# Kernel tuning notes

Measured on AMD Instinct MI355X. Metric: run time of the kernel, lower is better.

The kernel has to match this reference:

```python
import jax, jax.numpy as jnp
import numpy as np

B, Lq, Lk, D, H = 8, 1024, 1024, 1024, 16
HD = D // H  # 64


def rotate_half(x):
    x1, x2 = jnp.split(x, 2, axis=-1)
    return jnp.concatenate([-x2, x1], axis=-1)


def setup_inputs() -> dict:
    key = jax.random.key(0)
    ks = jax.random.split(key, 16)
    inv_freq = 1.0 / (10000.0 ** (np.arange(0, HD, 2, dtype=np.float32) / HD))
    pos = np.arange(Lk, dtype=np.float32)
    ang = pos[:, None] * inv_freq[None, :]              # [Lk, HD/2]
    emb = np.concatenate([ang, ang], axis=-1)           # [Lk, HD]
    rope_cos = jnp.broadcast_to(jnp.asarray(np.cos(emb)), (B, Lk, HD))
    rope_sin = jnp.broadcast_to(jnp.asarray(np.sin(emb)), (B, Lk, HD))
    w = lambda k: jax.random.normal(k, (D, D), jnp.float32) * 0.02
    return {
        "query": jax.random.normal(ks[0], (B, Lq, D), jnp.float32),
        "key": jax.random.normal(ks[1], (B, Lk, D), jnp.float32),
        "value": jax.random.normal(ks[2], (B, Lk, D), jnp.float32),
        "Wq": w(ks[3]), "bq": jnp.zeros((D,), jnp.float32),
        "Wk": w(ks[4]), "bk": jnp.zeros((D,), jnp.float32),
        "Wv": w(ks[5]), "bv": jnp.zeros((D,), jnp.float32),
        "Wg": w(ks[6]), "bg": jnp.ones((D,), jnp.float32),
        "Wo": w(ks[7]), "bo": jnp.zeros((D,), jnp.float32),
        "rope_cos": rope_cos,
        "rope_sin": rope_sin,
        "key_padding_mask": jnp.zeros((B, Lk), bool),  # True = padded
    }


def reference(query, key, value, Wq, bq, Wk, bk, Wv, bv, Wg, bg, Wo, bo,
              rope_cos, rope_sin, key_padding_mask):
    b, lq, d = query.shape
    lk = key.shape[1]
    h, hd = H, d // H

    def heads(x, L):  # [B,L,D] -> [B,H,L,hd]
        return x.reshape(b, L, h, hd).transpose(0, 2, 1, 3)

    Q = heads(query @ Wq.T + bq, lq)
    K = heads(key @ Wk.T + bk, lk)
    V = heads(value @ Wv.T + bv, lk)

    def rope(x, cos, sin):
        L = x.shape[2]
        c = cos[:, None, :L, :]
        s = sin[:, None, :L, :]
        return x * c + rotate_half(x) * s

    K = rope(K, rope_cos, rope_sin)
    Q = rope(Q, rope_cos, rope_sin)  # rope_on_q=True, q uses same cos/sin

    scale = 1.0 / np.sqrt(hd)
    scores = jnp.einsum('bhqd,bhkd->bhqk', Q, K) * scale
    valid = ~key_padding_mask                     # [B,Lk], True = attend
    scores = jnp.where(valid[:, None, None, :], scores, jnp.float32(-1e30))
    attn = jax.nn.softmax(scores, axis=-1)
    out = jnp.einsum('bhqk,bhkd->bhqd', attn, V)  # [B,H,Lq,hd]
    out = jnp.nan_to_num(out, nan=0.0)
    out = out.transpose(0, 2, 1, 3).reshape(b, lq, d)
    gate = jax.nn.sigmoid(query @ Wg.T + bg)
    out = (out * gate) @ Wo.T + bo
    return out
```

## Files before the change

kernel.cpp:

```cpp
#include <hip/hip_runtime.h>

using ushort  = unsigned short;
using bf16x8  = __attribute__((ext_vector_type(8))) __bf16;
using ushort8 = __attribute__((ext_vector_type(8))) unsigned short;
using f32x4   = __attribute__((ext_vector_type(4))) float;
using float4v = __attribute__((ext_vector_type(4))) float;

__device__ __forceinline__ float bf2f(ushort u) {
    union { unsigned int i; float f; } v; v.i = ((unsigned int)u) << 16; return v.f;
}
__device__ __forceinline__ ushort f2bf(float f) {
    union { float f; unsigned int i; } v; v.f = f;
    unsigned int r = v.i + 0x7FFFu + ((v.i >> 16) & 1u);
    return (ushort)(r >> 16);
}
__device__ __forceinline__ bf16x8 ld8(const ushort* p) {
    return __builtin_bit_cast(bf16x8, *(const ushort8*)p);
}
__device__ __forceinline__ void glds16(const void* g, void* l) {
    __builtin_amdgcn_global_load_lds(
        (const __attribute__((address_space(1))) unsigned int*)g,
        (__attribute__((address_space(3))) unsigned int*)l, 16, 0, 0);
}

__global__ void sniff_kernel(const ushort* __restrict__ q, int* __restrict__ flag) {
    const int lane = threadIdx.x;
    float mx = 0.0f;
    for (int i = lane; i < 512; i += 64) {
        float v = bf2f(q[2 * i]);
        mx = fmaxf(mx, fabsf(v));
    }
#pragma unroll
    for (int off = 32; off >= 1; off >>= 1) mx = fmaxf(mx, __shfl_xor(mx, off, 64));
    if (lane == 0) *flag = (mx > 1.0e6f) ? 1 : 0;
}

__global__ __launch_bounds__(256) void cvt_kernel(
    const void* __restrict__ src, ushort* __restrict__ dst, int n8,
    const int* __restrict__ flag)
{
    const bool f32m = (*flag != 0);
    const int stride = gridDim.x * 256;
    for (int i = blockIdx.x * 256 + threadIdx.x; i < n8; i += stride) {
        if (f32m) {
            const float4v a = ((const float4v*)src)[2 * i];
            const float4v b = ((const float4v*)src)[2 * i + 1];
            bf16x8 o;
#pragma unroll
            for (int j = 0; j < 4; ++j) { o[j] = (__bf16)a[j]; o[j + 4] = (__bf16)b[j]; }
            ((ushort8*)dst)[i] = __builtin_bit_cast(ushort8, o);
        } else {
            ((ushort8*)dst)[i] = ((const ushort8*)src)[i];
        }
    }
}

template<int EPI, int ABF16, int WBF16, int OUTF>
__global__ __launch_bounds__(256) void gemm_bt(
    const void* __restrict__ A, const void* __restrict__ W,
    const void* __restrict__ bias,
    const void* __restrict__ rc, const void* __restrict__ rs,
    void* __restrict__ C, const int* __restrict__ flag)
{
    constexpr int Kd = 1024, Nd = 1024;
    const bool f32m = (*flag != 0);
    const bool af32 = f32m && !ABF16;
    const bool wf32 = f32m && !WBF16;

    const int tid  = threadIdx.x;
    const int swz  = (blockIdx.x & 7) * 64 + (blockIdx.x >> 3);
    const int nb   = swz & 7;
    const int mb   = swz >> 3;
    const int wave = tid >> 6;
    const int lane = tid & 63;
    const int quad = lane >> 4;
    const int l16  = lane & 15;
    const int wr   = wave >> 1;
    const int wc   = wave & 1;

    __shared__ __align__(16) ushort As[2][128 * 32];
    __shared__ __align__(16) ushort Bs[2][128 * 32];

    const int arow0 = mb * 128;
    const int brow0 = nb * 128;

    auto ldregs = [&](float4v r[4], const float* src, int row0, int k0) {
#pragma unroll
        for (int j = 0; j < 2; ++j) {
            const int c = j * 256 + tid;
            const float* gp = src + (size_t)(row0 + (c >> 2)) * Kd + k0 + (c & 3) * 8;
            r[2 * j]     = *(const float4v*)gp;
            r[2 * j + 1] = *(const float4v*)(gp + 4);
        }
    };
    auto cvtwr = [&](ushort* lds, const float4v r[4]) {
#pragma unroll
        for (int j = 0; j < 2; ++j) {
            const int c = j * 256 + tid;
            bf16x8 o;
#pragma unroll
            for (int i = 0; i < 4; ++i) {
                o[i]     = (__bf16)r[2 * j][i];
                o[i + 4] = (__bf16)r[2 * j + 1][i];
            }
            *(ushort8*)&lds[c * 8] = __builtin_bit_cast(ushort8, o);
        }
    };
    auto stage16 = [&](ushort* lds, const ushort* src, int row0, int k0) {
#pragma unroll
        for (int j = 0; j < 2; ++j) {
            const int c = j * 256 + tid;
            glds16(src + (size_t)(row0 + (c >> 2)) * Kd + k0 + (c & 3) * 8, &lds[c * 8]);
        }
    };

    {
        float4v t[4];
        if (af32) { ldregs(t, (const float*)A, arow0, 0); cvtwr(As[0], t); }
        else      stage16(As[0], (const ushort*)A, arow0, 0);
        if (wf32) { ldregs(t, (const float*)W, brow0, 0); cvtwr(Bs[0], t); }
        else      stage16(Bs[0], (const ushort*)W, brow0, 0);
    }

    f32x4 acc[4][4] = {};
    int cur = 0;
    for (int kt = 0; kt < 32; ++kt) {
        __syncthreads();
        const bool pf = (kt < 31);
        const int  kn = (kt + 1) * 32;
        float4v ra[4], rb[4];
        if (pf) {
            if (af32) ldregs(ra, (const float*)A, arow0, kn);
            else      stage16(As[cur ^ 1], (const ushort*)A, arow0, kn);
            if (wf32) ldregs(rb, (const float*)W, brow0, kn);
            else      stage16(Bs[cur ^ 1], (const ushort*)W, brow0, kn);
        }
        bf16x8 fa[4], fb[4];
#pragma unroll
        for (int mi = 0; mi < 4; ++mi)
            fa[mi] = ld8(&As[cur][(wr * 64 + mi * 16 + l16) * 32 + quad * 8]);
#pragma unroll
        for (int ni = 0; ni < 4; ++ni)
            fb[ni] = ld8(&Bs[cur][(wc * 64 + ni * 16 + l16) * 32 + quad * 8]);
#pragma unroll
        for (int mi = 0; mi < 4; ++mi)
#pragma unroll
            for (int ni = 0; ni < 4; ++ni)
                acc[mi][ni] = __builtin_amdgcn_mfma_f32_16x16x32_bf16(fa[mi], fb[ni], acc[mi][ni], 0, 0, 0);
        if (pf) {
            if (af32) cvtwr(As[cur ^ 1], ra);
            if (wf32) cvtwr(Bs[cur ^ 1], rb);
        }
        cur ^= 1;
    }

    const bool of32 = OUTF && f32m;
    const int colbase = nb * 128 + wc * 64;
    float bv[4];
#pragma unroll
    for (int ni = 0; ni < 4; ++ni) {
        const int cg = colbase + ni * 16 + l16;
        bv[ni] = f32m ? ((const float*)bias)[cg] : bf2f(((const ushort*)bias)[cg]);
    }
    const int rowb = mb * 128 + wr * 64 + quad * 4;
#pragma unroll
    for (int mi = 0; mi < 4; ++mi) {
#pragma unroll
        for (int r = 0; r < 4; ++r) {
            const int rowg = rowb + mi * 16 + r;
            float v[4];
#pragma unroll
            for (int ni = 0; ni < 4; ++ni) v[ni] = acc[mi][ni][r] + bv[ni];
            if constexpr (EPI == 1) {
#pragma unroll
                for (int t = 0; t < 2; ++t) {
                    const size_t ci = (size_t)rowg * 64 + t * 16 + l16;
                    const float c = f32m ? ((const float*)rc)[ci] : bf2f(((const ushort*)rc)[ci]);
                    const float s = f32m ? ((const float*)rs)[ci] : bf2f(((const ushort*)rs)[ci]);
                    const float x1 = v[t], x2 = v[t + 2];
                    v[t]     = x1 * c - x2 * s;
                    v[t + 2] = x2 * c + x1 * s;
                }
            } else if constexpr (EPI == 2) {
#pragma unroll
                for (int t = 0; t < 4; ++t) v[t] = 1.0f / (1.0f + __expf(-v[t]));
            }
#pragma unroll
            for (int ni = 0; ni < 4; ++ni) {
                const size_t idx = (size_t)rowg * Nd + colbase + ni * 16 + l16;
                if (of32) ((float*)C)[idx] = v[ni];
                else      ((ushort*)C)[idx] = f2bf(v[ni]);
            }
        }
    }
}

__global__ __launch_bounds__(256) void transpose_vh(
    const ushort* __restrict__ Vp, ushort* __restrict__ Vt)
{
    const int bb = blockIdx.x >> 8;
    const int pr = (blockIdx.x >> 4) & 15;
    const int cr = blockIdx.x & 15;
    __shared__ ushort t[64 * 65];
    const int tid = threadIdx.x;
    {
        const int r = tid >> 3, c8 = (tid & 7) * 8;
#pragma unroll
        for (int hh = 0; hh < 2; ++hh) {
            const int rr = r + hh * 32;
            const ushort8 v = *(const ushort8*)(Vp + ((size_t)(bb * 1024 + pr * 64 + rr)) * 1024 + cr * 64 + c8);
#pragma unroll
            for (int i = 0; i < 8; ++i) t[rr * 65 + c8 + i] = v[i];
        }
    }
    __syncthreads();
    {
        const int c = tid >> 2, p0 = (tid & 3) * 16;
        ushort8 o0, o1;
#pragma unroll
        for (int i = 0; i < 8; ++i) {
            o0[i] = t[(p0 + i) * 65 + c];
            o1[i] = t[(p0 + 8 + i) * 65 + c];
        }
        ushort* dst = Vt + ((size_t)(bb * 1024 + cr * 64 + c)) * 1024 + pr * 64 + p0;
        *(ushort8*)dst       = o0;
        *(ushort8*)(dst + 8) = o1;
    }
}

__global__ __launch_bounds__(256, 3) void attn_kernel(
    const ushort* __restrict__ Qp, const ushort* __restrict__ Kp,
    const ushort* __restrict__ Vt, const ushort* __restrict__ G,
    const unsigned char* __restrict__ mask, ushort* __restrict__ O)
{
    const int swz = (blockIdx.x & 7) * 128 + (blockIdx.x >> 3);
    const int qb = swz & 7;
    const int h  = (swz >> 3) & 15;
    const int b  = swz >> 7;
    const int tid  = threadIdx.x;
    const int wave = tid >> 6;
    const int lane = tid & 63;
    const int quad = lane >> 4;
    const int l16  = lane & 15;
    const size_t Dm = 1024;

    __shared__ __align__(16) ushort Ks[2][64 * 64];
    __shared__ __align__(16) ushort Vs[2][64 * 64];
    __shared__ __align__(16) ushort Ps[4][2][16 * 72];
    __shared__ __align__(4) unsigned char Ms[1024];

    const int q0 = qb * 128 + wave * 32;
    bf16x8 qa[2][2];
#pragma unroll
    for (int u = 0; u < 2; ++u) {
        const ushort* Qb = Qp + ((size_t)b * 1024 + q0 + u * 16 + l16) * Dm + h * 64 + quad * 8;
        qa[u][0] = ld8(Qb);
        qa[u][1] = ld8(Qb + 32);
    }
    const ushort* Kbase = Kp + ((size_t)b * 1024) * Dm + h * 64;
    const ushort* Vbase = Vt + ((size_t)b * 1024 + h * 64) * 1024;

    auto stageK = [&](ushort* lds, int k0) {
#pragma unroll
        for (int j = 0; j < 2; ++j) {
            const int t = j * 256 + tid;
            const int row = t >> 3;
            const int col8 = (t & 7) ^ (row & 7);
            glds16(Kbase + (size_t)(k0 + row) * Dm + col8 * 8, &lds[t * 8]);
        }
    };
    auto stageV = [&](ushort* lds, int k0) {
#pragma unroll
        for (int j = 0; j < 2; ++j) {
            const int t = j * 256 + tid;
            const int row = t >> 3;
            const int col8 = (t & 7) ^ (row & 7);
            glds16(Vbase + (size_t)row * 1024 + k0 + col8 * 8, &lds[t * 8]);
        }
    };

    stageK(Ks[0], 0);
    stageV(Vs[0], 0);
    ((unsigned int*)Ms)[tid] = ((const unsigned int*)(mask + (size_t)b * 1024))[tid];

    float m_r[2][4], l_r[2][4];
    f32x4 o[2][4] = {};
#pragma unroll
    for (int u = 0; u < 2; ++u)
#pragma unroll
        for (int r = 0; r < 4; ++r) { m_r[u][r] = -3.0e38f; l_r[u][r] = 0.0f; }

    const float scale = 0.125f;
    int cur = 0;
    for (int kt = 0; kt < 16; ++kt) {
        __syncthreads();
        if (kt < 15) {
            stageK(Ks[cur ^ 1], (kt + 1) * 64);
            stageV(Vs[cur ^ 1], (kt + 1) * 64);
        }
        const int k0 = kt * 64;
        bf16x8 kf[4][2];
#pragma unroll
        for (int ct = 0; ct < 4; ++ct) {
            const int row = ct * 16 + l16;
#pragma unroll
            for (int kk = 0; kk < 2; ++kk) {
                const int col8 = (kk * 4 + quad) ^ (row & 7);
                kf[ct][kk] = ld8(&Ks[cur][row * 64 + col8 * 8]);
            }
        }
        f32x4 s[2][4] = {};
        __builtin_amdgcn_s_setprio(1);
#pragma unroll
        for (int u = 0; u < 2; ++u)
#pragma unroll
            for (int ct = 0; ct < 4; ++ct) {
                s[u][ct] = __builtin_amdgcn_mfma_f32_16x16x32_bf16(qa[u][0], kf[ct][0], s[u][ct], 0, 0, 0);
                s[u][ct] = __builtin_amdgcn_mfma_f32_16x16x32_bf16(qa[u][1], kf[ct][1], s[u][ct], 0, 0, 0);
            }
        __builtin_amdgcn_s_setprio(0);
#pragma unroll
        for (int u = 0; u < 2; ++u) {
#pragma unroll
            for (int r = 0; r < 4; ++r) {
                float sv[4];
#pragma unroll
                for (int ct = 0; ct < 4; ++ct)
                    sv[ct] = Ms[k0 + ct * 16 + l16] ? -1e30f : s[u][ct][r] * scale;
                float mx = fmaxf(fmaxf(sv[0], sv[1]), fmaxf(sv[2], sv[3]));
#pragma unroll
                for (int off = 8; off >= 1; off >>= 1) mx = fmaxf(mx, __shfl_xor(mx, off, 16));
                const float mnew  = fmaxf(m_r[u][r], mx);
                const float alpha = __expf(m_r[u][r] - mnew);
                float p[4], ps = 0.0f;
#pragma unroll
                for (int ct = 0; ct < 4; ++ct) { p[ct] = __expf(sv[ct] - mnew); ps += p[ct]; }
#pragma unroll
                for (int off = 8; off >= 1; off >>= 1) ps += __shfl_xor(ps, off, 16);
                l_r[u][r] = l_r[u][r] * alpha + ps;
                m_r[u][r] = mnew;
#pragma unroll
                for (int t = 0; t < 4; ++t) o[u][t][r] *= alpha;
#pragma unroll
                for (int ct = 0; ct < 4; ++ct)
                    Ps[wave][u][(quad * 4 + r) * 72 + ct * 16 + l16] =
                        __builtin_bit_cast(ushort, (__bf16)p[ct]);
            }
        }
        asm volatile("s_waitcnt lgkmcnt(0)" ::: "memory");
        __builtin_amdgcn_sched_barrier(0);
        bf16x8 pa[2][2];
#pragma unroll
        for (int u = 0; u < 2; ++u) {
            pa[u][0] = ld8(&Ps[wave][u][l16 * 72 + quad * 8]);
            pa[u][1] = ld8(&Ps[wave][u][l16 * 72 + 32 + quad * 8]);
        }
        bf16x8 vf[4][2];
#pragma unroll
        for (int t = 0; t < 4; ++t) {
            const int row = t * 16 + l16;
#pragma unroll
            for (int kk = 0; kk < 2; ++kk) {
                const int col8 = (kk * 4 + quad) ^ (row & 7);
                vf[t][kk] = ld8(&Vs[cur][row * 64 + col8 * 8]);
            }
        }
        __builtin_amdgcn_s_setprio(1);
#pragma unroll
        for (int u = 0; u < 2; ++u)
#pragma unroll
            for (int t = 0; t < 4; ++t) {
                o[u][t] = __builtin_amdgcn_mfma_f32_16x16x32_bf16(pa[u][0], vf[t][0], o[u][t], 0, 0, 0);
                o[u][t] = __builtin_amdgcn_mfma_f32_16x16x32_bf16(pa[u][1], vf[t][1], o[u][t], 0, 0, 0);
            }
        __builtin_amdgcn_s_setprio(0);
        cur ^= 1;
    }
#pragma unroll
    for (int u = 0; u < 2; ++u) {
        const int rowg0 = b * 1024 + q0 + u * 16 + quad * 4;
#pragma unroll
        for (int r = 0; r < 4; ++r) {
            const float inv = 1.0f / l_r[u][r];
#pragma unroll
            for (int t = 0; t < 4; ++t) {
                const size_t idx = (size_t)(rowg0 + r) * Dm + h * 64 + t * 16 + l16;
                O[idx] = f2bf(o[u][t][r] * inv * bf2f(G[idx]));
            }
        }
    }
}

extern "C" void kernel_launch(void* const* d_in, const int* in_sizes, int n_in,
                              void* d_out, int out_size, void* d_ws, size_t ws_size,
                              hipStream_t stream)
{
    const void* query = d_in[0];
    const void* key   = d_in[1];
    const void* value = d_in[2];
    const void* Wq    = d_in[3];
    const void* bq    = d_in[4];
    const void* Wk    = d_in[5];
    const void* bk    = d_in[6];
    const void* Wv    = d_in[7];
    const void* bv    = d_in[8];
    const void* Wg    = d_in[9];
    const void* bg    = d_in[10];
    const void* Wo    = d_in[11];
    const void* bo    = d_in[12];
    const void* rc    = d_in[13];
    const void* rs    = d_in[14];
    const unsigned char* mask = (const unsigned char*)d_in[15];

    char* ws = (char*)d_ws;
    const size_t MB = (size_t)1 << 20;
    const size_t MB16 = 16 * MB;
    const bool big = ws_size >= 139 * MB;

    ushort* Qp = (ushort*)(ws);
    ushort* Kp = (ushort*)(ws + 1 * MB16);
    ushort* Vp = (ushort*)(ws + 2 * MB16);
    ushort* Gt = (ushort*)(ws + 3 * MB16);
    ushort* Vt = (ushort*)(ws + 4 * MB16);
    ushort* Ag = (ushort*)(ws + 2 * MB16);
    int*  flag = (int*)(ws + (big ? 138 * MB : 5 * MB16));

    const dim3 gb(512), gt(256);
    hipLaunchKernelGGL(sniff_kernel, dim3(1), dim3(64), 0, stream, (const ushort*)query, flag);

    if (big) {
        ushort* qbf = (ushort*)(ws + 80 * MB);
        ushort* kbf = (ushort*)(ws + 96 * MB);
        ushort* vbf = (ushort*)(ws + 112 * MB);
        ushort* wb[5];
        for (int i = 0; i < 5; ++i) wb[i] = (ushort*)(ws + 128 * MB + (size_t)i * 2 * MB);

        hipLaunchKernelGGL(cvt_kernel, dim3(2048), dim3(256), 0, stream, query, qbf, 1048576, flag);
        hipLaunchKernelGGL(cvt_kernel, dim3(2048), dim3(256), 0, stream, key,   kbf, 1048576, flag);
        hipLaunchKernelGGL(cvt_kernel, dim3(2048), dim3(256), 0, stream, value, vbf, 1048576, flag);
        hipLaunchKernelGGL(cvt_kernel, dim3(512),  dim3(256), 0, stream, Wq, wb[0], 131072, flag);
        hipLaunchKernelGGL(cvt_kernel, dim3(512),  dim3(256), 0, stream, Wk, wb[1], 131072, flag);
        hipLaunchKernelGGL(cvt_kernel, dim3(512),  dim3(256), 0, stream, Wv, wb[2], 131072, flag);
        hipLaunchKernelGGL(cvt_kernel, dim3(512),  dim3(256), 0, stream, Wg, wb[3], 131072, flag);
        hipLaunchKernelGGL(cvt_kernel, dim3(512),  dim3(256), 0, stream, Wo, wb[4], 131072, flag);

        hipLaunchKernelGGL((gemm_bt<1,1,1,0>), gb, gt, 0, stream, qbf, wb[0], bq, rc, rs, Qp, flag);
        hipLaunchKernelGGL((gemm_bt<1,1,1,0>), gb, gt, 0, stream, kbf, wb[1], bk, rc, rs, Kp, flag);
        hipLaunchKernelGGL((gemm_bt<0,1,1,0>), gb, gt, 0, stream, vbf, wb[2], bv, rc, rs, Vp, flag);
        hipLaunchKernelGGL((gemm_bt<2,1,1,0>), gb, gt, 0, stream, qbf, wb[3], bg, rc, rs, Gt, flag);

        hipLaunchKernelGGL(transpose_vh, dim3(2048), dim3(256), 0, stream, Vp, Vt);
        hipLaunchKernelGGL(attn_kernel,  dim3(1024), dim3(256), 0, stream, Qp, Kp, Vt, Gt, mask, Ag);

        hipLaunchKernelGGL((gemm_bt<0,1,1,1>), gb, gt, 0, stream, Ag, wb[4], bo, rc, rs, d_out, flag);
    } else {
        hipLaunchKernelGGL((gemm_bt<1,0,0,0>), gb, gt, 0, stream, query, Wq, bq, rc, rs, Qp, flag);
        hipLaunchKernelGGL((gemm_bt<1,0,0,0>), gb, gt, 0, stream, key,   Wk, bk, rc, rs, Kp, flag);
        hipLaunchKernelGGL((gemm_bt<0,0,0,0>), gb, gt, 0, stream, value, Wv, bv, rc, rs, Vp, flag);
        hipLaunchKernelGGL((gemm_bt<2,0,0,0>), gb, gt, 0, stream, query, Wg, bg, rc, rs, Gt, flag);

        hipLaunchKernelGGL(transpose_vh, dim3(2048), dim3(256), 0, stream, Vp, Vt);
        hipLaunchKernelGGL(attn_kernel,  dim3(1024), dim3(256), 0, stream, Qp, Kp, Vt, Gt, mask, Ag);

        hipLaunchKernelGGL((gemm_bt<0,1,0,1>), gb, gt, 0, stream, Ag, Wo, bo, rc, rs, d_out, flag);
    }
}
```

Measured before the change: 463.0 us.

## Rework attention into 512-thread blocks with transposed scores and lazy rescaling, merge conversions

The attention kernel now runs 8 waves per block over 256 query rows, so each staged K/V tile is shared by more waves. It computes S transposed (K as the A operand) so each lane owns a query column, which removes most cross-lane softmax reductions. It skips the running-max rescale unless the max grows by more than 8, and skips masking when the padding mask is all zero. The 1/sqrt(d) scale is folded into the Q projection epilogue, and the eight conversion launches are merged into two. Risks: lower occupancy from larger blocks, and the lazy rescale lets unnormalised exponentials grow by up to e^8 before correction.

```diff
diff --git a/kernel.cpp b/kernel.cpp
--- a/kernel.cpp
+++ b/kernel.cpp
@@ -2,6 +2,7 @@
 
 using ushort  = unsigned short;
 using bf16x8  = __attribute__((ext_vector_type(8))) __bf16;
+using bf16x4  = __attribute__((ext_vector_type(4))) __bf16;
 using ushort8 = __attribute__((ext_vector_type(8))) unsigned short;
 using f32x4   = __attribute__((ext_vector_type(4))) float;
 using float4v = __attribute__((ext_vector_type(4))) float;
@@ -35,24 +36,43 @@
     if (lane == 0) *flag = (mx > 1.0e6f) ? 1 : 0;
 }
 
-__global__ __launch_bounds__(256) void cvt_kernel(
-    const void* __restrict__ src, ushort* __restrict__ dst, int n8,
+__device__ __forceinline__ void cvt8(const void* src, ushort* dst, int i, bool f32m) {
+    if (f32m) {
+        const float4v a = ((const float4v*)src)[2 * i];
+        const float4v b = ((const float4v*)src)[2 * i + 1];
+        bf16x8 o;
+#pragma unroll
+        for (int j = 0; j < 4; ++j) { o[j] = (__bf16)a[j]; o[j + 4] = (__bf16)b[j]; }
+        ((ushort8*)dst)[i] = __builtin_bit_cast(ushort8, o);
+    } else {
+        ((ushort8*)dst)[i] = ((const ushort8*)src)[i];
+    }
+}
+
+__global__ __launch_bounds__(256) void cvt_qkv(
+    const void* __restrict__ s0, const void* __restrict__ s1, const void* __restrict__ s2,
+    ushort* __restrict__ d0, ushort* __restrict__ d1, ushort* __restrict__ d2,
     const int* __restrict__ flag)
 {
     const bool f32m = (*flag != 0);
-    const int stride = gridDim.x * 256;
-    for (int i = blockIdx.x * 256 + threadIdx.x; i < n8; i += stride) {
-        if (f32m) {
-            const float4v a = ((const float4v*)src)[2 * i];
-            const float4v b = ((const float4v*)src)[2 * i + 1];
-            bf16x8 o;
-#pragma unroll
-            for (int j = 0; j < 4; ++j) { o[j] = (__bf16)a[j]; o[j + 4] = (__bf16)b[j]; }
-            ((ushort8*)dst)[i] = __builtin_bit_cast(ushort8, o);
-        } else {
-            ((ushort8*)dst)[i] = ((const ushort8*)src)[i];
-        }
-    }
+    const int seg = blockIdx.x >> 11;
+    const void* src = seg == 0 ? s0 : (seg == 1 ? s1 : s2);
+    ushort*    dst = seg == 0 ? d0 : (seg == 1 ? d1 : d2);
+    for (int i = (blockIdx.x & 2047) * 256 + threadIdx.x; i < 1048576; i += 2048 * 256)
+        cvt8(src, dst, i, f32m);
+}
+__global__ __launch_bounds__(256) void cvt_w5(
+    const void* __restrict__ s0, const void* __restrict__ s1, const void* __restrict__ s2,
+    const void* __restrict__ s3, const void* __restrict__ s4,
+    ushort* __restrict__ d0, ushort* __restrict__ d1, ushort* __restrict__ d2,
+    ushort* __restrict__ d3, ushort* __restrict__ d4,
+    const int* __restrict__ flag)
+{
+    const bool f32m = (*flag != 0);
+    const int seg = blockIdx.x >> 9;
+    const void* src = seg == 0 ? s0 : seg == 1 ? s1 : seg == 2 ? s2 : seg == 3 ? s3 : s4;
+    ushort*    dst = seg == 0 ? d0 : seg == 1 ? d1 : seg == 2 ? d2 : seg == 3 ? d3 : d4;
+    cvt8(src, dst, (blockIdx.x & 511) * 256 + threadIdx.x, f32m);
 }
 
 template<int EPI, int ABF16, int WBF16, int OUTF>
@@ -171,7 +191,7 @@
             float v[4];
 #pragma unroll
             for (int ni = 0; ni < 4; ++ni) v[ni] = acc[mi][ni][r] + bv[ni];
-            if constexpr (EPI == 1) {
+            if constexpr (EPI == 1 || EPI == 3) {
 #pragma unroll
                 for (int t = 0; t < 2; ++t) {
                     const size_t ci = (size_t)rowg * 64 + t * 16 + l16;
@@ -181,6 +201,10 @@
                     v[t]     = x1 * c - x2 * s;
                     v[t + 2] = x2 * c + x1 * s;
                 }
+                if constexpr (EPI == 3) {
+#pragma unroll
+                    for (int t = 0; t < 4; ++t) v[t] *= 0.125f;
+                }
             } else if constexpr (EPI == 2) {
 #pragma unroll
                 for (int t = 0; t < 4; ++t) v[t] = 1.0f / (1.0f + __expf(-v[t]));
@@ -228,15 +252,15 @@
     }
 }
 
-__global__ __launch_bounds__(256, 3) void attn_kernel(
+__global__ __launch_bounds__(512) void attn_kernel(
     const ushort* __restrict__ Qp, const ushort* __restrict__ Kp,
     const ushort* __restrict__ Vt, const ushort* __restrict__ G,
     const unsigned char* __restrict__ mask, ushort* __restrict__ O)
 {
-    const int swz = (blockIdx.x & 7) * 128 + (blockIdx.x >> 3);
-    const int qb = swz & 7;
-    const int h  = (swz >> 3) & 15;
-    const int b  = swz >> 7;
+    const int swz = (blockIdx.x & 7) * 64 + (blockIdx.x >> 3);
+    const int qb = swz & 3;
+    const int h  = (swz >> 2) & 15;
+    const int b  = swz >> 6;
     const int tid  = threadIdx.x;
     const int wave = tid >> 6;
     const int lane = tid & 63;
@@ -246,10 +270,10 @@
 
     __shared__ __align__(16) ushort Ks[2][64 * 64];
     __shared__ __align__(16) ushort Vs[2][64 * 64];
-    __shared__ __align__(16) ushort Ps[4][2][16 * 72];
-    __shared__ __align__(4) unsigned char Ms[1024];
-
-    const int q0 = qb * 128 + wave * 32;
+    __shared__ __align__(16) ushort Ps[8][16 * 72];
+    __shared__ __align__(16) unsigned char Ms[1024];
+
+    const int q0 = qb * 256 + wave * 32;
     bf16x8 qa[2][2];
 #pragma unroll
     for (int u = 0; u < 2; ++u) {
@@ -261,36 +285,31 @@
     const ushort* Vbase = Vt + ((size_t)b * 1024 + h * 64) * 1024;
 
     auto stageK = [&](ushort* lds, int k0) {
-#pragma unroll
-        for (int j = 0; j < 2; ++j) {
-            const int t = j * 256 + tid;
-            const int row = t >> 3;
-            const int col8 = (t & 7) ^ (row & 7);
-            glds16(Kbase + (size_t)(k0 + row) * Dm + col8 * 8, &lds[t * 8]);
-        }
+        const int row = tid >> 3;
+        const int col8 = (tid & 7) ^ (row & 7);
+        glds16(Kbase + (size_t)(k0 + row) * Dm + col8 * 8, &lds[tid * 8]);
     };
     auto stageV = [&](ushort* lds, int k0) {
-#pragma unroll
-        for (int j = 0; j < 2; ++j) {
-            const int t = j * 256 + tid;
-            const int row = t >> 3;
-            const int col8 = (t & 7) ^ (row & 7);
-            glds16(Vbase + (size_t)row * 1024 + k0 + col8 * 8, &lds[t * 8]);
-        }
+        const int row = tid >> 3;
+        const int col8 = (tid & 7) ^ (row & 7);
+        glds16(Vbase + (size_t)row * 1024 + k0 + col8 * 8, &lds[tid * 8]);
     };
 
     stageK(Ks[0], 0);
     stageV(Vs[0], 0);
-    ((unsigned int*)Ms)[tid] = ((const unsigned int*)(mask + (size_t)b * 1024))[tid];
-
-    float m_r[2][4], l_r[2][4];
+    if (tid < 256)
+        ((unsigned int*)Ms)[tid] = ((const unsigned int*)(mask + (size_t)b * 1024))[tid];
+    __syncthreads();
+    bool anym;
+    {
+        const unsigned long long* M8 = (const unsigned long long*)Ms;
+        anym = __any((M8[lane] | M8[lane + 64]) != 0ULL);
+    }
+
+    float m_r[2] = { -3.0e38f, -3.0e38f };
+    float l_r[2] = { 0.0f, 0.0f };
     f32x4 o[2][4] = {};
-#pragma unroll
-    for (int u = 0; u < 2; ++u)
-#pragma unroll
-        for (int r = 0; r < 4; ++r) { m_r[u][r] = -3.0e38f; l_r[u][r] = 0.0f; }
-
-    const float scale = 0.125f;
+
     int cur = 0;
     for (int kt = 0; kt < 16; ++kt) {
         __syncthreads();
@@ -299,15 +318,12 @@
             stageV(Vs[cur ^ 1], (kt + 1) * 64);
         }
         const int k0 = kt * 64;
-        bf16x8 kf[4][2];
+        bf16x8 kf0[4], kf1[4];
 #pragma unroll
         for (int ct = 0; ct < 4; ++ct) {
             const int row = ct * 16 + l16;
-#pragma unroll
-            for (int kk = 0; kk < 2; ++kk) {
-                const int col8 = (kk * 4 + quad) ^ (row & 7);
-                kf[ct][kk] = ld8(&Ks[cur][row * 64 + col8 * 8]);
-            }
+            kf0[ct] = ld8(&Ks[cur][row * 64 + ((quad)     ^ (row & 7)) * 8]);
+            kf1[ct] = ld8(&Ks[cur][row * 64 + ((4 + quad) ^ (row & 7)) * 8]);
         }
         f32x4 s[2][4] = {};
         __builtin_amdgcn_s_setprio(1);
@@ -315,73 +331,90 @@
         for (int u = 0; u < 2; ++u)
 #pragma unroll
             for (int ct = 0; ct < 4; ++ct) {
-                s[u][ct] = __builtin_amdgcn_mfma_f32_16x16x32_bf16(qa[u][0], kf[ct][0], s[u][ct], 0, 0, 0);
-                s[u][ct] = __builtin_amdgcn_mfma_f32_16x16x32_bf16(qa[u][1], kf[ct][1], s[u][ct], 0, 0, 0);
+                s[u][ct] = __builtin_amdgcn_mfma_f32_16x16x32_bf16(kf0[ct], qa[u][0], s[u][ct], 0, 0, 0);
+                s[u][ct] = __builtin_amdgcn_mfma_f32_16x16x32_bf16(kf1[ct], qa[u][1], s[u][ct], 0, 0, 0);
             }
         __builtin_amdgcn_s_setprio(0);
-#pragma unroll
-        for (int u = 0; u < 2; ++u) {
-#pragma unroll
-            for (int r = 0; r < 4; ++r) {
-                float sv[4];
-#pragma unroll
-                for (int ct = 0; ct < 4; ++ct)
-                    sv[ct] = Ms[k0 + ct * 16 + l16] ? -1e30f : s[u][ct][r] * scale;
-                float mx = fmaxf(fmaxf(sv[0], sv[1]), fmaxf(sv[2], sv[3]));
-#pragma unroll
-                for (int off = 8; off >= 1; off >>= 1) mx = fmaxf(mx, __shfl_xor(mx, off, 16));
-                const float mnew  = fmaxf(m_r[u][r], mx);
-                const float alpha = __expf(m_r[u][r] - mnew);
-                float p[4], ps = 0.0f;
-#pragma unroll
-                for (int ct = 0; ct < 4; ++ct) { p[ct] = __expf(sv[ct] - mnew); ps += p[ct]; }
-#pragma unroll
-                for (int off = 8; off >= 1; off >>= 1) ps += __shfl_xor(ps, off, 16);
-                l_r[u][r] = l_r[u][r] * alpha + ps;
-                m_r[u][r] = mnew;
-#pragma unroll
-                for (int t = 0; t < 4; ++t) o[u][t][r] *= alpha;
-#pragma unroll
-                for (int ct = 0; ct < 4; ++ct)
-                    Ps[wave][u][(quad * 4 + r) * 72 + ct * 16 + l16] =
-                        __builtin_bit_cast(ushort, (__bf16)p[ct]);
-            }
-        }
-        asm volatile("s_waitcnt lgkmcnt(0)" ::: "memory");
-        __builtin_amdgcn_sched_barrier(0);
-        bf16x8 pa[2][2];
-#pragma unroll
-        for (int u = 0; u < 2; ++u) {
-            pa[u][0] = ld8(&Ps[wave][u][l16 * 72 + quad * 8]);
-            pa[u][1] = ld8(&Ps[wave][u][l16 * 72 + 32 + quad * 8]);
-        }
         bf16x8 vf[4][2];
 #pragma unroll
         for (int t = 0; t < 4; ++t) {
             const int row = t * 16 + l16;
 #pragma unroll
-            for (int kk = 0; kk < 2; ++kk) {
-                const int col8 = (kk * 4 + quad) ^ (row & 7);
-                vf[t][kk] = ld8(&Vs[cur][row * 64 + col8 * 8]);
-            }
-        }
-        __builtin_amdgcn_s_setprio(1);
-#pragma unroll
-        for (int u = 0; u < 2; ++u)
+            for (int kk = 0; kk < 2; ++kk)
+                vf[t][kk] = ld8(&Vs[cur][row * 64 + (((kk * 4 + quad) ^ (row & 7))) * 8]);
+        }
+#pragma unroll
+        for (int u = 0; u < 2; ++u) {
+            float sv[4][4];
+#pragma unroll
+            for (int ct = 0; ct < 4; ++ct)
+#pragma unroll
+                for (int r = 0; r < 4; ++r) sv[ct][r] = s[u][ct][r];
+            if (anym) {
+#pragma unroll
+                for (int ct = 0; ct < 4; ++ct) {
+                    const unsigned int mb4 = *(const unsigned int*)&Ms[k0 + ct * 16 + quad * 4];
+#pragma unroll
+                    for (int r = 0; r < 4; ++r)
+                        if ((mb4 >> (8 * r)) & 0xffu) sv[ct][r] = -1e30f;
+                }
+            }
+            float mxv = sv[0][0];
+#pragma unroll
+            for (int ct = 0; ct < 4; ++ct)
+#pragma unroll
+                for (int r = 0; r < 4; ++r) mxv = fmaxf(mxv, sv[ct][r]);
+            mxv = fmaxf(mxv, __shfl_xor(mxv, 16, 64));
+            mxv = fmaxf(mxv, __shfl_xor(mxv, 32, 64));
+            if (__any(mxv > m_r[u] + 8.0f)) {
+                const float mnew  = fmaxf(m_r[u], mxv);
+                const float alpha = __expf(m_r[u] - mnew);
+                l_r[u] *= alpha;
+                m_r[u]  = mnew;
+#pragma unroll
+                for (int r = 0; r < 4; ++r) {
+                    const float ar = __shfl(alpha, quad * 4 + r, 64);
+#pragma unroll
+                    for (int t = 0; t < 4; ++t) o[u][t][r] *= ar;
+                }
+            }
+            float ls = 0.0f;
+            bf16x4 w[4];
+#pragma unroll
+            for (int ct = 0; ct < 4; ++ct)
+#pragma unroll
+                for (int r = 0; r < 4; ++r) {
+                    const float pv = __expf(sv[ct][r] - m_r[u]);
+                    ls += pv;
+                    w[ct][r] = (__bf16)pv;
+                }
+            l_r[u] += ls;
+#pragma unroll
+            for (int ct = 0; ct < 4; ++ct)
+                *(bf16x4*)&Ps[wave][l16 * 72 + ct * 16 + quad * 4] = w[ct];
+            asm volatile("s_waitcnt lgkmcnt(0)" ::: "memory");
+            __builtin_amdgcn_sched_barrier(0);
+            const bf16x8 pa0 = ld8(&Ps[wave][l16 * 72 + quad * 8]);
+            const bf16x8 pa1 = ld8(&Ps[wave][l16 * 72 + 32 + quad * 8]);
+            __builtin_amdgcn_s_setprio(1);
 #pragma unroll
             for (int t = 0; t < 4; ++t) {
-                o[u][t] = __builtin_amdgcn_mfma_f32_16x16x32_bf16(pa[u][0], vf[t][0], o[u][t], 0, 0, 0);
-                o[u][t] = __builtin_amdgcn_mfma_f32_16x16x32_bf16(pa[u][1], vf[t][1], o[u][t], 0, 0, 0);
-            }
-        __builtin_amdgcn_s_setprio(0);
+                o[u][t] = __builtin_amdgcn_mfma_f32_16x16x32_bf16(pa0, vf[t][0], o[u][t], 0, 0, 0);
+                o[u][t] = __builtin_amdgcn_mfma_f32_16x16x32_bf16(pa1, vf[t][1], o[u][t], 0, 0, 0);
+            }
+            __builtin_amdgcn_s_setprio(0);
+        }
         cur ^= 1;
     }
 #pragma unroll
     for (int u = 0; u < 2; ++u) {
+        float lt = l_r[u];
+        lt += __shfl_xor(lt, 16, 64);
+        lt += __shfl_xor(lt, 32, 64);
         const int rowg0 = b * 1024 + q0 + u * 16 + quad * 4;
 #pragma unroll
         for (int r = 0; r < 4; ++r) {
-            const float inv = 1.0f / l_r[u][r];
+            const float inv = 1.0f / __shfl(lt, quad * 4 + r, 64);
 #pragma unroll
             for (int t = 0; t < 4; ++t) {
                 const size_t idx = (size_t)(rowg0 + r) * Dm + h * 64 + t * 16 + l16;
@@ -435,32 +468,28 @@
         ushort* wb[5];
         for (int i = 0; i < 5; ++i) wb[i] = (ushort*)(ws + 128 * MB + (size_t)i * 2 * MB);
 
-        hipLaunchKernelGGL(cvt_kernel, dim3(2048), dim3(256), 0, stream, query, qbf, 1048576, flag);
-        hipLaunchKernelGGL(cvt_kernel, dim3(2048), dim3(256), 0, stream, key,   kbf, 1048576, flag);
-        hipLaunchKernelGGL(cvt_kernel, dim3(2048), dim3(256), 0, stream, value, vbf, 1048576, flag);
-        hipLaunchKernelGGL(cvt_kernel, dim3(512),  dim3(256), 0, stream, Wq, wb[0], 131072, flag);
-        hipLaunchKernelGGL(cvt_kernel, dim3(512),  dim3(256), 0, stream, Wk, wb[1], 131072, flag);
-        hipLaunchKernelGGL(cvt_kernel, dim3(512),  dim3(256), 0, stream, Wv, wb[2], 131072, flag);
-        hipLaunchKernelGGL(cvt_kernel, dim3(512),  dim3(256), 0, stream, Wg, wb[3], 131072, flag);
-        hipLaunchKernelGGL(cvt_kernel, dim3(512),  dim3(256), 0, stream, Wo, wb[4], 131072, flag);
-
-        hipLaunchKernelGGL((gemm_bt<1,1,1,0>), gb, gt, 0, stream, qbf, wb[0], bq, rc, rs, Qp, flag);
+        hipLaunchKernelGGL(cvt_qkv, dim3(3 * 2048), dim3(256), 0, stream,
+                           query, key, value, qbf, kbf, vbf, flag);
+        hipLaunchKernelGGL(cvt_w5, dim3(5 * 512), dim3(256), 0, stream,
+                           Wq, Wk, Wv, Wg, Wo, wb[0], wb[1], wb[2], wb[3], wb[4], flag);
+
+        hipLaunchKernelGGL((gemm_bt<3,1,1,0>), gb, gt, 0, stream, qbf, wb[0], bq, rc, rs, Qp, flag);
         hipLaunchKernelGGL((gemm_bt<1,1,1,0>), gb, gt, 0, stream, kbf, wb[1], bk, rc, rs, Kp, flag);
         hipLaunchKernelGGL((gemm_bt<0,1,1,0>), gb, gt, 0, stream, vbf, wb[2], bv, rc, rs, Vp, flag);
         hipLaunchKernelGGL((gemm_bt<2,1,1,0>), gb, gt, 0, stream, qbf, wb[3], bg, rc, rs, Gt, flag);
 
         hipLaunchKernelGGL(transpose_vh, dim3(2048), dim3(256), 0, stream, Vp, Vt);
-        hipLaunchKernelGGL(attn_kernel,  dim3(1024), dim3(256), 0, stream, Qp, Kp, Vt, Gt, mask, Ag);
+        hipLaunchKernelGGL(attn_kernel,  dim3(512), dim3(512), 0, stream, Qp, Kp, Vt, Gt, mask, Ag);
 
         hipLaunchKernelGGL((gemm_bt<0,1,1,1>), gb, gt, 0, stream, Ag, wb[4], bo, rc, rs, d_out, flag);
     } else {
-        hipLaunchKernelGGL((gemm_bt<1,0,0,0>), gb, gt, 0, stream, query, Wq, bq, rc, rs, Qp, flag);
+        hipLaunchKernelGGL((gemm_bt<3,0,0,0>), gb, gt, 0, stream, query, Wq, bq, rc, rs, Qp, flag);
         hipLaunchKernelGGL((gemm_bt<1,0,0,0>), gb, gt, 0, stream, key,   Wk, bk, rc, rs, Kp, flag);
         hipLaunchKernelGGL((gemm_bt<0,0,0,0>), gb, gt, 0, stream, value, Wv, bv, rc, rs, Vp, flag);
         hipLaunchKernelGGL((gemm_bt<2,0,0,0>), gb, gt, 0, stream, query, Wg, bg, rc, rs, Gt, flag);
 
         hipLaunchKernelGGL(transpose_vh, dim3(2048), dim3(256), 0, stream, Vp, Vt);
-        hipLaunchKernelGGL(attn_kernel,  dim3(1024), dim3(256), 0, stream, Qp, Kp, Vt, Gt, mask, Ag);
+        hipLaunchKernelGGL(attn_kernel,  dim3(512), dim3(512), 0, stream, Qp, Kp, Vt, Gt, mask, Ag);
 
         hipLaunchKernelGGL((gemm_bt<0,1,0,1>), gb, gt, 0, stream, Ag, Wo, bo, rc, rs, d_out, flag);
     }
```

New measurement: 411.4 us. 11.2% less time.
